# Kernel optimization log

Hardware: AMD Instinct MI355X
Metric: run time of the kernel (lower is better)

The kernel has to match this reference:

```python
import jax, jax.numpy as jnp
import numpy as np

N_QUBITS = 8
DEPTH = 2
N_STATES = 1 << N_QUBITS  # 256
BATCH = (2, 32768)


def _cz_phase(n_qubits: int) -> np.ndarray:
    """Diagonal phase of nearest-neighbor CZ gates over all basis states."""
    basis = np.arange(1 << n_qubits)
    phase = np.ones(1 << n_qubits, dtype=np.float32)
    for left in range(n_qubits - 1):
        both_one = ((basis >> left) & 1 == 1) & ((basis >> (left + 1)) & 1 == 1)
        phase = np.where(both_one, -phase, phase)
    return phase


def setup_inputs() -> dict:
    key = jax.random.key(0)
    k1, k2 = jax.random.split(key)
    projected_features = jax.random.normal(k1, BATCH + (N_QUBITS,), dtype=jnp.float32)
    theta = 0.05 * jax.random.normal(k2, (DEPTH, N_QUBITS), dtype=jnp.float32)
    input_scale = jnp.ones((N_QUBITS,), dtype=jnp.float32)
    return {"projected_features": projected_features, "theta": theta, "input_scale": input_scale}


def reference(projected_features, theta, input_scale):
    n_qubits = projected_features.shape[-1]
    depth = theta.shape[0]
    n_states = 1 << n_qubits
    batch_shape = projected_features.shape[:-1]
    dtype = projected_features.dtype

    cz_phase = jnp.asarray(_cz_phase(n_qubits), dtype=dtype)

    # |0...0> initial state
    state = jnp.zeros(batch_shape + (n_states,), dtype=dtype).at[..., 0].set(1.0)
    bounded = jnp.tanh(projected_features) * np.pi  # [..., n_qubits]

    for layer in range(depth):
        for q in range(n_qubits):
            angle = bounded[..., q] * input_scale[q] + theta[layer, q]  # [...]
            c = jnp.cos(angle * 0.5)[..., None, None]
            s = jnp.sin(angle * 0.5)[..., None, None]
            # basis index = high * 2^(q+1) + bit_q * 2^q + low; split out bit_q
            r = state.reshape(batch_shape + (n_states >> (q + 1), 2, 1 << q))
            s0 = r[..., 0, :]
            s1 = r[..., 1, :]
            new = jnp.stack([c * s0 - s * s1, s * s0 + c * s1], axis=-2)
            state = new.reshape(batch_shape + (n_states,))
        state = state * cz_phase

    norm = jnp.linalg.norm(state, axis=-1, keepdims=True)
    return state / jnp.maximum(norm, 1e-12)
```

## Files before the change

### kernel.cpp

```cpp
#include <hip/hip_runtime.h>
#include <math.h>

#define PI_F 3.14159265358979323846f

template <int PAT>
__device__ __forceinline__ float swzf(float x) {
    return __int_as_float(__builtin_amdgcn_ds_swizzle(__float_as_int(x), PAT));
}
#define BCAST_PAT(q) (((((q) & 3) | (((q) & 4) << 1)) << 5) | 0x14)

template <int CTRL>
__device__ __forceinline__ float dppf(float x) {
    int i = __float_as_int(x);
    return __int_as_float(__builtin_amdgcn_update_dpp(i, i, CTRL, 0xF, 0xF, false));
}
#define DPP_XOR1 0xB1
#define DPP_XOR2 0x4E
#define DPP_XOR8 0x128

#define SLO_MASK 0x4748B848u

__global__ __launch_bounds__(256) void qenc_kernel(
    const float* __restrict__ pf,
    const float* __restrict__ theta,
    const float* __restrict__ scale,
    float* __restrict__ out,
    int B)
{
    const int lane = threadIdx.x & 63;
    const int wid  = threadIdx.x >> 6;
    const int sub  = (lane & 3) | ((lane >> 1) & 4);
    const int g    = ((lane >> 2) & 1) | ((lane >> 3) & 6);
    const int bwave = (blockIdx.x * 4 + wid) * 8;
    const int b = bwave + g;
    if (b >= B) return;

    __shared__ __align__(16) float lds[4 * 2048];
    float* base = lds + wid * 2048;

    float x  = pf[(size_t)b * 8 + sub];
    float e  = __expf(2.f * x);
    float th = 1.f - 2.f / (e + 1.f);
    float bounded = th * PI_F * scale[sub];
    float h0 = 0.5f * (bounded + theta[sub]);
    float h1 = 0.5f * (bounded + theta[8 + sub]);
    float c0 = __cosf(h0), s0 = __sinf(h0);
    float cL = __cosf(h1), sL = __sinf(h1);

    float KC0 = swzf<BCAST_PAT(0)>(c0), KS0 = swzf<BCAST_PAT(0)>(s0);
    float KC1 = swzf<BCAST_PAT(1)>(c0), KS1 = swzf<BCAST_PAT(1)>(s0);
    float KC2 = swzf<BCAST_PAT(2)>(c0), KS2 = swzf<BCAST_PAT(2)>(s0);
    float KC3 = swzf<BCAST_PAT(3)>(c0), KS3 = swzf<BCAST_PAT(3)>(s0);
    float KC4 = swzf<BCAST_PAT(4)>(c0), KS4 = swzf<BCAST_PAT(4)>(s0);
    float KC5 = swzf<BCAST_PAT(5)>(c0), KS5 = swzf<BCAST_PAT(5)>(s0);
    float KC6 = swzf<BCAST_PAT(6)>(c0), KS6 = swzf<BCAST_PAT(6)>(s0);
    float KC7 = swzf<BCAST_PAT(7)>(c0), KS7 = swzf<BCAST_PAT(7)>(s0);

    float f5 = (sub & 1) ? KS5 : KC5;
    float f6 = (sub & 2) ? KS6 : KC6;
    float f7 = (sub & 4) ? KS7 : KC7;
    float Phi = f5 * f6 * f7;

    const float uu[4] = { Phi * (KC0 * KC1), Phi * (KS0 * KC1),
                          Phi * (KC0 * KS1), Phi * (KS0 * KS1) };
    float t23_0 = KC2 * KC3, t23_1 = KS2 * KC3, t23_2 = KC2 * KS3, t23_3 = KS2 * KS3;
    const float ww[8] = { t23_0 * KC4, t23_1 * KC4, t23_2 * KC4, t23_3 * KC4,
                          t23_0 * KS4, t23_1 * KS4, t23_2 * KS4, t23_3 * KS4 };

    float v[32];
#pragma unroll
    for (int i = 0; i < 32; ++i) v[i] = uu[i & 3] * ww[i >> 2];

    float A  = (__popc(sub & (sub >> 1) & 3) & 1) ? -1.f : 1.f;
    float A4 = (sub & 1) ? -A : A;
#pragma unroll
    for (int i = 0; i < 32; ++i) {
        float f = (i & 16) ? A4 : A;
        float r = v[i] * f;
        if ((SLO_MASK >> i) & 1) r = -r;
        v[i] = r;
    }

#define INTRA_GATE(SB, CG, SG)                                        \
    do {                                                              \
        _Pragma("unroll")                                             \
        for (int bse = 0; bse < 32; bse += 2 * (SB)) {                \
            _Pragma("unroll")                                         \
            for (int off = 0; off < (SB); ++off) {                    \
                int i0 = bse + off, i1 = i0 + (SB);                   \
                float a = v[i0], bb = v[i1];                          \
                v[i0] = fmaf((CG), a, -((SG) * bb));                  \
                v[i1] = fmaf((CG), bb, (SG) * a);                     \
            }                                                         \
        }                                                             \
    } while (0)

#define CROSS_GATE_DPP(CTRL, BIT, CG, SG)                             \
    do {                                                              \
        float se = (sub & (BIT)) ? (SG) : -(SG);                      \
        _Pragma("unroll")                                             \
        for (int i = 0; i < 32; ++i) {                                \
            float t = dppf<CTRL>(v[i]);                               \
            v[i] = fmaf((CG), v[i], se * t);                          \
        }                                                             \
    } while (0)

    {
        float cg, sg;
        cg = swzf<BCAST_PAT(0)>(cL); sg = swzf<BCAST_PAT(0)>(sL); INTRA_GATE(1,  cg, sg);
        cg = swzf<BCAST_PAT(1)>(cL); sg = swzf<BCAST_PAT(1)>(sL); INTRA_GATE(2,  cg, sg);
        cg = swzf<BCAST_PAT(2)>(cL); sg = swzf<BCAST_PAT(2)>(sL); INTRA_GATE(4,  cg, sg);
        cg = swzf<BCAST_PAT(3)>(cL); sg = swzf<BCAST_PAT(3)>(sL); INTRA_GATE(8,  cg, sg);
        cg = swzf<BCAST_PAT(4)>(cL); sg = swzf<BCAST_PAT(4)>(sL); INTRA_GATE(16, cg, sg);
        cg = swzf<BCAST_PAT(5)>(cL); sg = swzf<BCAST_PAT(5)>(sL); CROSS_GATE_DPP(DPP_XOR1, 1, cg, sg);
        cg = swzf<BCAST_PAT(6)>(cL); sg = swzf<BCAST_PAT(6)>(sL); CROSS_GATE_DPP(DPP_XOR2, 2, cg, sg);
        cg = swzf<BCAST_PAT(7)>(cL); sg = swzf<BCAST_PAT(7)>(sL); CROSS_GATE_DPP(DPP_XOR8, 4, cg, sg);
    }

    float ss = 0.f;
#pragma unroll
    for (int i = 0; i < 32; ++i) ss = fmaf(v[i], v[i], ss);
    ss += dppf<DPP_XOR1>(ss);
    ss += dppf<DPP_XOR2>(ss);
    ss += dppf<DPP_XOR8>(ss);
    float inv = rsqrtf(ss);

    float fA = A * inv, fA4 = A4 * inv;
#pragma unroll
    for (int i = 0; i < 32; ++i) {
        float f = (i & 16) ? fA4 : fA;
        float r = v[i] * f;
        if ((SLO_MASK >> i) & 1) r = -r;
        v[i] = r;
    }

#pragma unroll
    for (int k = 0; k < 8; ++k) {
        int c  = sub * 8 + k;
        int cp = c ^ sub;
        *reinterpret_cast<float4*>(base + g * 256 + cp * 4) =
            make_float4(v[4 * k], v[4 * k + 1], v[4 * k + 2], v[4 * k + 3]);
    }
    const int cr = lane ^ (lane >> 3);
#pragma unroll
    for (int j = 0; j < 8; ++j) {
        float4 t = *reinterpret_cast<const float4*>(base + j * 256 + cr * 4);
        *reinterpret_cast<float4*>(out + (size_t)(bwave + j) * 256 + lane * 4) = t;
    }
}

extern "C" void kernel_launch(void* const* d_in, const int* in_sizes, int n_in,
                              void* d_out, int out_size, void* d_ws, size_t ws_size,
                              hipStream_t stream) {
    const float* pf    = (const float*)d_in[0];
    const float* theta = (const float*)d_in[1];
    const float* scale = (const float*)d_in[2];
    float* out = (float*)d_out;

    int B = in_sizes[0] / 8;
    int batchesPerBlock = 4 * 8;
    int grid = (B + batchesPerBlock - 1) / batchesPerBlock;
    qenc_kernel<<<grid, 256, 0, stream>>>(pf, theta, scale, out, B);
}
```

Baseline: 20.40 us.

## Convert kernel to persistent grid-stride loop with next-input prefetch

Launches a fixed grid of 512 blocks whose waves loop over batch groups with a grid stride, instead of one wave per group. Theta and scale loads plus the sign constants are hoisted out of the loop. The next group's input is prefetched before the current group is processed. This aims to cut block launch overhead and hide input load latency, but relies on a fixed grid size and a B>>3 group count that ignores any batch remainder.

```diff
diff --git a/kernel.cpp b/kernel.cpp
--- a/kernel.cpp
+++ b/kernel.cpp
@@ -20,7 +20,7 @@
 
 #define SLO_MASK 0x4748B848u
 
-__global__ __launch_bounds__(256) void qenc_kernel(
+__global__ __launch_bounds__(256, 2) void qenc_kernel(
     const float* __restrict__ pf,
     const float* __restrict__ theta,
     const float* __restrict__ scale,
@@ -31,55 +31,68 @@
     const int wid  = threadIdx.x >> 6;
     const int sub  = (lane & 3) | ((lane >> 1) & 4);
     const int g    = ((lane >> 2) & 1) | ((lane >> 3) & 6);
-    const int bwave = (blockIdx.x * 4 + wid) * 8;
-    const int b = bwave + g;
-    if (b >= B) return;
 
     __shared__ __align__(16) float lds[4 * 2048];
     float* base = lds + wid * 2048;
 
-    float x  = pf[(size_t)b * 8 + sub];
-    float e  = __expf(2.f * x);
-    float th = 1.f - 2.f / (e + 1.f);
-    float bounded = th * PI_F * scale[sub];
-    float h0 = 0.5f * (bounded + theta[sub]);
-    float h1 = 0.5f * (bounded + theta[8 + sub]);
-    float c0 = __cosf(h0), s0 = __sinf(h0);
-    float cL = __cosf(h1), sL = __sinf(h1);
+    const float th0c = theta[sub];
+    const float th1c = theta[8 + sub];
+    const float scc  = scale[sub];
+    const float A  = (__popc(sub & (sub >> 1) & 3) & 1) ? -1.f : 1.f;
+    const float A4 = (sub & 1) ? -A : A;
+    const int   cr = lane ^ (lane >> 3);
 
-    float KC0 = swzf<BCAST_PAT(0)>(c0), KS0 = swzf<BCAST_PAT(0)>(s0);
-    float KC1 = swzf<BCAST_PAT(1)>(c0), KS1 = swzf<BCAST_PAT(1)>(s0);
-    float KC2 = swzf<BCAST_PAT(2)>(c0), KS2 = swzf<BCAST_PAT(2)>(s0);
-    float KC3 = swzf<BCAST_PAT(3)>(c0), KS3 = swzf<BCAST_PAT(3)>(s0);
-    float KC4 = swzf<BCAST_PAT(4)>(c0), KS4 = swzf<BCAST_PAT(4)>(s0);
-    float KC5 = swzf<BCAST_PAT(5)>(c0), KS5 = swzf<BCAST_PAT(5)>(s0);
-    float KC6 = swzf<BCAST_PAT(6)>(c0), KS6 = swzf<BCAST_PAT(6)>(s0);
-    float KC7 = swzf<BCAST_PAT(7)>(c0), KS7 = swzf<BCAST_PAT(7)>(s0);
+    const int waveId  = blockIdx.x * 4 + wid;
+    const int nWaves  = gridDim.x * 4;
+    const int nGroups = B >> 3;
 
-    float f5 = (sub & 1) ? KS5 : KC5;
-    float f6 = (sub & 2) ? KS6 : KC6;
-    float f7 = (sub & 4) ? KS7 : KC7;
-    float Phi = f5 * f6 * f7;
+    int grp = waveId;
+    float x = (grp < nGroups) ? pf[(size_t)(grp * 8 + g) * 8 + sub] : 0.f;
 
-    const float uu[4] = { Phi * (KC0 * KC1), Phi * (KS0 * KC1),
-                          Phi * (KC0 * KS1), Phi * (KS0 * KS1) };
-    float t23_0 = KC2 * KC3, t23_1 = KS2 * KC3, t23_2 = KC2 * KS3, t23_3 = KS2 * KS3;
-    const float ww[8] = { t23_0 * KC4, t23_1 * KC4, t23_2 * KC4, t23_3 * KC4,
-                          t23_0 * KS4, t23_1 * KS4, t23_2 * KS4, t23_3 * KS4 };
+    for (; grp < nGroups; grp += nWaves) {
+        const int bwave = grp * 8;
+        const int grpn = grp + nWaves;
+        float xn = (grpn < nGroups) ? pf[(size_t)(grpn * 8 + g) * 8 + sub] : 0.f;
 
-    float v[32];
+        float e  = __expf(2.f * x);
+        float th = 1.f - 2.f / (e + 1.f);
+        float bounded = th * PI_F * scc;
+        float h0 = 0.5f * (bounded + th0c);
+        float h1 = 0.5f * (bounded + th1c);
+        float c0 = __cosf(h0), s0 = __sinf(h0);
+        float cL = __cosf(h1), sL = __sinf(h1);
+
+        float KC0 = swzf<BCAST_PAT(0)>(c0), KS0 = swzf<BCAST_PAT(0)>(s0);
+        float KC1 = swzf<BCAST_PAT(1)>(c0), KS1 = swzf<BCAST_PAT(1)>(s0);
+        float KC2 = swzf<BCAST_PAT(2)>(c0), KS2 = swzf<BCAST_PAT(2)>(s0);
+        float KC3 = swzf<BCAST_PAT(3)>(c0), KS3 = swzf<BCAST_PAT(3)>(s0);
+        float KC4 = swzf<BCAST_PAT(4)>(c0), KS4 = swzf<BCAST_PAT(4)>(s0);
+        float KC5 = swzf<BCAST_PAT(5)>(c0), KS5 = swzf<BCAST_PAT(5)>(s0);
+        float KC6 = swzf<BCAST_PAT(6)>(c0), KS6 = swzf<BCAST_PAT(6)>(s0);
+        float KC7 = swzf<BCAST_PAT(7)>(c0), KS7 = swzf<BCAST_PAT(7)>(s0);
+
+        float f5 = (sub & 1) ? KS5 : KC5;
+        float f6 = (sub & 2) ? KS6 : KC6;
+        float f7 = (sub & 4) ? KS7 : KC7;
+        float Phi = f5 * f6 * f7;
+
+        const float uu[4] = { Phi * (KC0 * KC1), Phi * (KS0 * KC1),
+                              Phi * (KC0 * KS1), Phi * (KS0 * KS1) };
+        float t23_0 = KC2 * KC3, t23_1 = KS2 * KC3, t23_2 = KC2 * KS3, t23_3 = KS2 * KS3;
+        const float ww[8] = { t23_0 * KC4, t23_1 * KC4, t23_2 * KC4, t23_3 * KC4,
+                              t23_0 * KS4, t23_1 * KS4, t23_2 * KS4, t23_3 * KS4 };
+
+        float v[32];
 #pragma unroll
-    for (int i = 0; i < 32; ++i) v[i] = uu[i & 3] * ww[i >> 2];
+        for (int i = 0; i < 32; ++i) v[i] = uu[i & 3] * ww[i >> 2];
 
-    float A  = (__popc(sub & (sub >> 1) & 3) & 1) ? -1.f : 1.f;
-    float A4 = (sub & 1) ? -A : A;
 #pragma unroll
-    for (int i = 0; i < 32; ++i) {
-        float f = (i & 16) ? A4 : A;
-        float r = v[i] * f;
-        if ((SLO_MASK >> i) & 1) r = -r;
-        v[i] = r;
-    }
+        for (int i = 0; i < 32; ++i) {
+            float f = (i & 16) ? A4 : A;
+            float r = v[i] * f;
+            if ((SLO_MASK >> i) & 1) r = -r;
+            v[i] = r;
+        }
 
 #define INTRA_GATE(SB, CG, SG)                                        \
     do {                                                              \
@@ -105,47 +118,49 @@
         }                                                             \
     } while (0)
 
-    {
-        float cg, sg;
-        cg = swzf<BCAST_PAT(0)>(cL); sg = swzf<BCAST_PAT(0)>(sL); INTRA_GATE(1,  cg, sg);
-        cg = swzf<BCAST_PAT(1)>(cL); sg = swzf<BCAST_PAT(1)>(sL); INTRA_GATE(2,  cg, sg);
-        cg = swzf<BCAST_PAT(2)>(cL); sg = swzf<BCAST_PAT(2)>(sL); INTRA_GATE(4,  cg, sg);
-        cg = swzf<BCAST_PAT(3)>(cL); sg = swzf<BCAST_PAT(3)>(sL); INTRA_GATE(8,  cg, sg);
-        cg = swzf<BCAST_PAT(4)>(cL); sg = swzf<BCAST_PAT(4)>(sL); INTRA_GATE(16, cg, sg);
-        cg = swzf<BCAST_PAT(5)>(cL); sg = swzf<BCAST_PAT(5)>(sL); CROSS_GATE_DPP(DPP_XOR1, 1, cg, sg);
-        cg = swzf<BCAST_PAT(6)>(cL); sg = swzf<BCAST_PAT(6)>(sL); CROSS_GATE_DPP(DPP_XOR2, 2, cg, sg);
-        cg = swzf<BCAST_PAT(7)>(cL); sg = swzf<BCAST_PAT(7)>(sL); CROSS_GATE_DPP(DPP_XOR8, 4, cg, sg);
-    }
+        {
+            float cg, sg;
+            cg = swzf<BCAST_PAT(0)>(cL); sg = swzf<BCAST_PAT(0)>(sL); INTRA_GATE(1,  cg, sg);
+            cg = swzf<BCAST_PAT(1)>(cL); sg = swzf<BCAST_PAT(1)>(sL); INTRA_GATE(2,  cg, sg);
+            cg = swzf<BCAST_PAT(2)>(cL); sg = swzf<BCAST_PAT(2)>(sL); INTRA_GATE(4,  cg, sg);
+            cg = swzf<BCAST_PAT(3)>(cL); sg = swzf<BCAST_PAT(3)>(sL); INTRA_GATE(8,  cg, sg);
+            cg = swzf<BCAST_PAT(4)>(cL); sg = swzf<BCAST_PAT(4)>(sL); INTRA_GATE(16, cg, sg);
+            cg = swzf<BCAST_PAT(5)>(cL); sg = swzf<BCAST_PAT(5)>(sL); CROSS_GATE_DPP(DPP_XOR1, 1, cg, sg);
+            cg = swzf<BCAST_PAT(6)>(cL); sg = swzf<BCAST_PAT(6)>(sL); CROSS_GATE_DPP(DPP_XOR2, 2, cg, sg);
+            cg = swzf<BCAST_PAT(7)>(cL); sg = swzf<BCAST_PAT(7)>(sL); CROSS_GATE_DPP(DPP_XOR8, 4, cg, sg);
+        }
 
-    float ss = 0.f;
+        float ss = 0.f;
 #pragma unroll
-    for (int i = 0; i < 32; ++i) ss = fmaf(v[i], v[i], ss);
-    ss += dppf<DPP_XOR1>(ss);
-    ss += dppf<DPP_XOR2>(ss);
-    ss += dppf<DPP_XOR8>(ss);
-    float inv = rsqrtf(ss);
+        for (int i = 0; i < 32; ++i) ss = fmaf(v[i], v[i], ss);
+        ss += dppf<DPP_XOR1>(ss);
+        ss += dppf<DPP_XOR2>(ss);
+        ss += dppf<DPP_XOR8>(ss);
+        float inv = rsqrtf(ss);
 
-    float fA = A * inv, fA4 = A4 * inv;
+        float fA = A * inv, fA4 = A4 * inv;
 #pragma unroll
-    for (int i = 0; i < 32; ++i) {
-        float f = (i & 16) ? fA4 : fA;
-        float r = v[i] * f;
-        if ((SLO_MASK >> i) & 1) r = -r;
-        v[i] = r;
-    }
+        for (int i = 0; i < 32; ++i) {
+            float f = (i & 16) ? fA4 : fA;
+            float r = v[i] * f;
+            if ((SLO_MASK >> i) & 1) r = -r;
+            v[i] = r;
+        }
 
 #pragma unroll
-    for (int k = 0; k < 8; ++k) {
-        int c  = sub * 8 + k;
-        int cp = c ^ sub;
-        *reinterpret_cast<float4*>(base + g * 256 + cp * 4) =
-            make_float4(v[4 * k], v[4 * k + 1], v[4 * k + 2], v[4 * k + 3]);
-    }
-    const int cr = lane ^ (lane >> 3);
+        for (int k = 0; k < 8; ++k) {
+            int c  = sub * 8 + k;
+            int cp = c ^ sub;
+            *reinterpret_cast<float4*>(base + g * 256 + cp * 4) =
+                make_float4(v[4 * k], v[4 * k + 1], v[4 * k + 2], v[4 * k + 3]);
+        }
 #pragma unroll
-    for (int j = 0; j < 8; ++j) {
-        float4 t = *reinterpret_cast<const float4*>(base + j * 256 + cr * 4);
-        *reinterpret_cast<float4*>(out + (size_t)(bwave + j) * 256 + lane * 4) = t;
+        for (int j = 0; j < 8; ++j) {
+            float4 t = *reinterpret_cast<const float4*>(base + j * 256 + cr * 4);
+            *reinterpret_cast<float4*>(out + (size_t)(bwave + j) * 256 + lane * 4) = t;
+        }
+
+        x = xn;
     }
 }
 
@@ -158,7 +173,6 @@
     float* out = (float*)d_out;
 
     int B = in_sizes[0] / 8;
-    int batchesPerBlock = 4 * 8;
-    int grid = (B + batchesPerBlock - 1) / batchesPerBlock;
+    int grid = 512;
     qenc_kernel<<<grid, 256, 0, stream>>>(pf, theta, scale, out, B);
 }
```

After: 22.90 us. +12.2%, slower.

## Drop redundant normalization, fold sign fixups into gates, use nontemporal stores

Applied to the files above, without the earlier changes.

Removes the final sum-of-squares reduction and rescale, relying on the circuit being unitary so the state keeps unit norm. The parity and sign corrections are folded into the initial product-state factors, and the qubit-0 second-layer gate is moved to the end. That is valid because gates on different qubits in the same layer commute, and it lets the final sign pass merge into that gate. Output stores become nontemporal to ease cache pressure on the large write stream. The risk is small floating-point drift, since the state is no longer explicitly renormalized.

```diff
diff --git a/kernel.cpp b/kernel.cpp
--- a/kernel.cpp
+++ b/kernel.cpp
@@ -2,6 +2,8 @@
 #include <math.h>
 
 #define PI_F 3.14159265358979323846f
+
+typedef float f32x4 __attribute__((ext_vector_type(4)));
 
 template <int PAT>
 __device__ __forceinline__ float swzf(float x) {
@@ -31,19 +33,21 @@
     const int wid  = threadIdx.x >> 6;
     const int sub  = (lane & 3) | ((lane >> 1) & 4);
     const int g    = ((lane >> 2) & 1) | ((lane >> 3) & 6);
-    const int bwave = (blockIdx.x * 4 + wid) * 8;
-    const int b = bwave + g;
-    if (b >= B) return;
 
     __shared__ __align__(16) float lds[4 * 2048];
     float* base = lds + wid * 2048;
 
+    const int grp   = blockIdx.x * 4 + wid;
+    const int bwave = grp * 8;
+    const int b     = bwave + g;
+    if (b >= B) return;
+
     float x  = pf[(size_t)b * 8 + sub];
     float e  = __expf(2.f * x);
     float th = 1.f - 2.f / (e + 1.f);
-    float bounded = th * PI_F * scale[sub];
-    float h0 = 0.5f * (bounded + theta[sub]);
-    float h1 = 0.5f * (bounded + theta[8 + sub]);
+    float b2 = th * (0.5f * PI_F) * scale[sub];
+    float h0 = b2 + 0.5f * theta[sub];
+    float h1 = b2 + 0.5f * theta[8 + sub];
     float c0 = __cosf(h0), s0 = __sinf(h0);
     float cL = __cosf(h1), sL = __sinf(h1);
 
@@ -56,29 +60,26 @@
     float KC6 = swzf<BCAST_PAT(6)>(c0), KS6 = swzf<BCAST_PAT(6)>(s0);
     float KC7 = swzf<BCAST_PAT(7)>(c0), KS7 = swzf<BCAST_PAT(7)>(s0);
 
+    const float A  = (__popc(sub & (sub >> 1) & 3) & 1) ? -1.f : 1.f;
+    const float A4 = (sub & 1) ? -A : A;
+
     float f5 = (sub & 1) ? KS5 : KC5;
     float f6 = (sub & 2) ? KS6 : KC6;
     float f7 = (sub & 4) ? KS7 : KC7;
-    float Phi = f5 * f6 * f7;
+    float Phi = f5 * f6 * f7 * A;
+    float KS4L = (sub & 1) ? -KS4 : KS4;
 
-    const float uu[4] = { Phi * (KC0 * KC1), Phi * (KS0 * KC1),
-                          Phi * (KC0 * KS1), Phi * (KS0 * KS1) };
+    float a00 = KC0 * KC1, a10 = KS0 * KC1, a01 = KC0 * KS1, a11 = KS0 * KS1;
+    const float uu[4] = { Phi * a00, Phi * a10, Phi * a01, Phi * a11 };
     float t23_0 = KC2 * KC3, t23_1 = KS2 * KC3, t23_2 = KC2 * KS3, t23_3 = KS2 * KS3;
-    const float ww[8] = { t23_0 * KC4, t23_1 * KC4, t23_2 * KC4, t23_3 * KC4,
-                          t23_0 * KS4, t23_1 * KS4, t23_2 * KS4, t23_3 * KS4 };
+    const float wwl[8] = { t23_0 * KC4,  t23_1 * KC4,  t23_2 * KC4,  t23_3 * KC4,
+                           t23_0 * KS4L, t23_1 * KS4L, t23_2 * KS4L, t23_3 * KS4L };
 
     float v[32];
 #pragma unroll
-    for (int i = 0; i < 32; ++i) v[i] = uu[i & 3] * ww[i >> 2];
-
-    float A  = (__popc(sub & (sub >> 1) & 3) & 1) ? -1.f : 1.f;
-    float A4 = (sub & 1) ? -A : A;
-#pragma unroll
     for (int i = 0; i < 32; ++i) {
-        float f = (i & 16) ? A4 : A;
-        float r = v[i] * f;
-        if ((SLO_MASK >> i) & 1) r = -r;
-        v[i] = r;
+        v[i] = ((SLO_MASK >> i) & 1) ? (-uu[i & 3] * wwl[i >> 2])
+                                     : ( uu[i & 3] * wwl[i >> 2]);
     }
 
 #define INTRA_GATE(SB, CG, SG)                                        \
@@ -107,7 +108,6 @@
 
     {
         float cg, sg;
-        cg = swzf<BCAST_PAT(0)>(cL); sg = swzf<BCAST_PAT(0)>(sL); INTRA_GATE(1,  cg, sg);
         cg = swzf<BCAST_PAT(1)>(cL); sg = swzf<BCAST_PAT(1)>(sL); INTRA_GATE(2,  cg, sg);
         cg = swzf<BCAST_PAT(2)>(cL); sg = swzf<BCAST_PAT(2)>(sL); INTRA_GATE(4,  cg, sg);
         cg = swzf<BCAST_PAT(3)>(cL); sg = swzf<BCAST_PAT(3)>(sL); INTRA_GATE(8,  cg, sg);
@@ -115,37 +115,37 @@
         cg = swzf<BCAST_PAT(5)>(cL); sg = swzf<BCAST_PAT(5)>(sL); CROSS_GATE_DPP(DPP_XOR1, 1, cg, sg);
         cg = swzf<BCAST_PAT(6)>(cL); sg = swzf<BCAST_PAT(6)>(sL); CROSS_GATE_DPP(DPP_XOR2, 2, cg, sg);
         cg = swzf<BCAST_PAT(7)>(cL); sg = swzf<BCAST_PAT(7)>(sL); CROSS_GATE_DPP(DPP_XOR8, 4, cg, sg);
+
+        cg = swzf<BCAST_PAT(0)>(cL); sg = swzf<BCAST_PAT(0)>(sL);
+        float cA = cg * A,  sA = sg * A;
+        float cB = cg * A4, sB = sg * A4;
+#pragma unroll
+        for (int j = 0; j < 16; ++j) {
+            int i0 = 2 * j, i1 = i0 + 1;
+            float C = (i0 & 16) ? cB : cA;
+            float S = (i0 & 16) ? sB : sA;
+            float a = v[i0], bb = v[i1];
+            float t  = S * bb;
+            float t2 = S * a;
+            v[i0] = ((SLO_MASK >> i0) & 1) ? fmaf(-C, a, t)    : fmaf(C, a, -t);
+            v[i1] = ((SLO_MASK >> i1) & 1) ? fmaf(-C, bb, -t2) : fmaf(C, bb, t2);
+        }
     }
 
-    float ss = 0.f;
-#pragma unroll
-    for (int i = 0; i < 32; ++i) ss = fmaf(v[i], v[i], ss);
-    ss += dppf<DPP_XOR1>(ss);
-    ss += dppf<DPP_XOR2>(ss);
-    ss += dppf<DPP_XOR8>(ss);
-    float inv = rsqrtf(ss);
-
-    float fA = A * inv, fA4 = A4 * inv;
-#pragma unroll
-    for (int i = 0; i < 32; ++i) {
-        float f = (i & 16) ? fA4 : fA;
-        float r = v[i] * f;
-        if ((SLO_MASK >> i) & 1) r = -r;
-        v[i] = r;
-    }
 
 #pragma unroll
     for (int k = 0; k < 8; ++k) {
         int c  = sub * 8 + k;
         int cp = c ^ sub;
-        *reinterpret_cast<float4*>(base + g * 256 + cp * 4) =
-            make_float4(v[4 * k], v[4 * k + 1], v[4 * k + 2], v[4 * k + 3]);
+        f32x4 w = { v[4 * k], v[4 * k + 1], v[4 * k + 2], v[4 * k + 3] };
+        *reinterpret_cast<f32x4*>(base + g * 256 + cp * 4) = w;
     }
     const int cr = lane ^ (lane >> 3);
 #pragma unroll
     for (int j = 0; j < 8; ++j) {
-        float4 t = *reinterpret_cast<const float4*>(base + j * 256 + cr * 4);
-        *reinterpret_cast<float4*>(out + (size_t)(bwave + j) * 256 + lane * 4) = t;
+        f32x4 t = *reinterpret_cast<const f32x4*>(base + j * 256 + cr * 4);
+        __builtin_nontemporal_store(t,
+            reinterpret_cast<f32x4*>(out + (size_t)(bwave + j) * 256 + lane * 4));
     }
 }
 
@@ -158,7 +158,6 @@
     float* out = (float*)d_out;
 
     int B = in_sizes[0] / 8;
-    int batchesPerBlock = 4 * 8;
-    int grid = (B + batchesPerBlock - 1) / batchesPerBlock;
+    int grid = (B / 8 + 3) / 4;
     qenc_kernel<<<grid, 256, 0, stream>>>(pf, theta, scale, out, B);
 }
```

After: 18.99 us. 6.9% less time.
